# Kernel tuning notes

Hardware: AMD Instinct MI355X
Metric: run time of the kernel (lower is better)

The kernel has to match this reference:

```python
import jax, jax.numpy as jnp
import numpy as np

ROI_SIZE = 7
MAX_BIN_H = 8   # max adaptive-maxpool bin height for crop H <= 37
MAX_BIN_W = 9   # max adaptive-maxpool bin width  for crop W <= 50
SCALE = 0.0625  # 1/16 feature stride


def setup_inputs() -> dict:
    key = jax.random.key(0)
    ks = jax.random.split(key, 12)
    B, C, h, w = 1, 512, 37, 50          # conv5 feature map of a 600x800 image
    N = 512                               # number of ROIs (proposals)
    n_class = 21
    d_in, d_fc = C * ROI_SIZE * ROI_SIZE, 4096
    x = jax.random.normal(ks[0], (B, C, h, w), dtype=jnp.float32)
    # rois in image coordinates (x1, y1, x2, y2), image is 800x600
    x1 = jax.random.uniform(ks[1], (N,), minval=0.0, maxval=700.0)
    y1 = jax.random.uniform(ks[2], (N,), minval=0.0, maxval=500.0)
    bw = jax.random.uniform(ks[3], (N,), minval=16.0, maxval=400.0)
    bh = jax.random.uniform(ks[4], (N,), minval=16.0, maxval=300.0)
    rois = jnp.stack([x1, y1, jnp.minimum(x1 + bw, 799.0), jnp.minimum(y1 + bh, 599.0)], axis=1).astype(jnp.float32)
    roi_index = jnp.zeros((N,), dtype=jnp.int32)  # single image in batch
    W1 = jax.random.normal(ks[5], (d_in, d_fc), dtype=jnp.float32) * 0.01
    b1 = jnp.zeros((d_fc,), dtype=jnp.float32)
    W2 = jax.random.normal(ks[6], (d_fc, d_fc), dtype=jnp.float32) * 0.01
    b2 = jnp.zeros((d_fc,), dtype=jnp.float32)
    Wp = jax.random.normal(ks[7], (d_fc, n_class * 4), dtype=jnp.float32) * 0.001
    bp = jax.random.normal(ks[8], (n_class * 4,), dtype=jnp.float32) * 0.001
    Ws = jax.random.normal(ks[9], (d_fc, n_class), dtype=jnp.float32) * 0.01
    bs = jax.random.normal(ks[10], (n_class,), dtype=jnp.float32) * 0.01
    return dict(x=x, rois=rois, roi_index=roi_index, W1=W1, b1=b1, W2=W2, b2=b2, Wp=Wp, bp=bp, Ws=Ws, bs=bs)


def _roi_pool(x, rois, roi_index):
    """Faithful port of roi_pooling(): per-ROI crop + AdaptiveMaxPool2d(7)."""
    B, C, h, w = x.shape
    S = ROI_SIZE
    coords = jnp.round(rois * SCALE)  # round-half-even, like torch.round
    cx1 = jnp.clip(coords[:, 0], 0, w).astype(jnp.int32)
    cy1 = jnp.clip(coords[:, 1], 0, h).astype(jnp.int32)
    cx2 = jnp.clip(coords[:, 2], 0, w).astype(jnp.int32)
    cy2 = jnp.clip(coords[:, 3], 0, h).astype(jnp.int32)
    bidx = roi_index.astype(jnp.int32)
    roi_stack = jnp.stack([bidx, cx1, cy1, cx2, cy2], axis=1)  # [N,5]

    def pool_one(carry, roi):
        bi, x1i, y1i, x2i, y2i = roi[0], roi[1], roi[2], roi[3], roi[4]
        valid = (x1i < x2i) & (y1i < y2i)
        # torch slicing roi[2]:roi[4]+1 silently truncates at the tensor edge
        x2e = jnp.minimum(x2i, w - 1)
        y2e = jnp.minimum(y2i, h - 1)
        Hc = y2e - y1i + 1
        Wc = x2e - x1i + 1
        i = jnp.arange(S)
        # adaptive max pool bins: [floor(i*H/S), ceil((i+1)*H/S))
        rs = y1i + (i * Hc) // S
        re = y1i + ((i + 1) * Hc + S - 1) // S
        cs = x1i + (i * Wc) // S
        ce = x1i + ((i + 1) * Wc + S - 1) // S
        rows = rs[:, None] + jnp.arange(MAX_BIN_H)          # [S, MBH]
        rmask = rows < re[:, None]
        rows = jnp.clip(rows, 0, h - 1)
        cols = cs[:, None] + jnp.arange(MAX_BIN_W)          # [S, MBW]
        cmask = cols < ce[:, None]
        cols = jnp.clip(cols, 0, w - 1)
        feat = x[bi]                                         # [C, h, w]
        g = feat[:, rows[:, None, :, None], cols[None, :, None, :]]  # [C,S,S,MBH,MBW]
        mask = rmask[:, None, :, None] & cmask[None, :, None, :]     # [S,S,MBH,MBW]
        pooled = jnp.where(mask, g, -jnp.inf).max(axis=(-2, -1))    # [C,S,S]
        pooled = jnp.where(valid, pooled, jnp.zeros_like(pooled))
        return carry, pooled

    _, out = jax.lax.scan(pool_one, None, roi_stack)  # [N, C, S, S]
    return out


def reference(x, rois, roi_index, W1, b1, W2, b2, Wp, bp, Ws, bs):
    pooled = _roi_pool(x, rois, roi_index)            # [N, 512, 7, 7]
    flat = pooled.reshape(pooled.shape[0], -1)        # [N, 25088]
    fc6 = jax.nn.relu(flat @ W1 + b1)                 # [N, 4096]
    fc7 = jax.nn.relu(fc6 @ W2 + b2)                  # [N, 4096]
    roi_class_params = fc7 @ Wp + bp                  # [N, n_class*4]
    roi_scores = fc7 @ Ws + bs                        # [N, n_class]
    return (roi_class_params, roi_scores)
```

## Files before the change

### kernel.cpp

```cpp
#include <hip/hip_runtime.h>
#include <hip/hip_bf16.h>

using f32x4  = float          __attribute__((ext_vector_type(4)));
using bf16x8 = __bf16         __attribute__((ext_vector_type(8)));
using u16x8  = unsigned short __attribute__((ext_vector_type(8)));

#define C_CH 512
#define H_IN 37
#define W_IN 50
#define NPOS 1850
#define NROI 512
#define DIN  25088
#define DFC  4096
#define NPAR 84
#define NCLS 21
#define KS_FC 4
#define KS_HEAD 16

#define PB_X  232
#define PB_WH 2048
#define PB_TOT (PB_X + PB_WH)

__device__ __forceinline__ unsigned pack_bf16x2(float a, float b) {
    __hip_bfloat162 h;
    h.x = __float2bfloat16(a);
    h.y = __float2bfloat16(b);
    return *reinterpret_cast<unsigned*>(&h);
}

__global__ __launch_bounds__(256) void prep_kernel(
        const float* __restrict__ x, float* __restrict__ xt,
        const float* __restrict__ Wp, const float* __restrict__ Ws,
        float* __restrict__ Whp) {
    __shared__ float tile[64][65];
    int b = blockIdx.x;
    int t = threadIdx.x;
    if (b < PB_X) {
        int p0 = (b % 29) * 64;
        int c0 = (b / 29) * 64;
        int tc = t & 63, tr = t >> 6;
#pragma unroll
        for (int i = 0; i < 16; ++i) {
            int r = tr + i * 4;
            int p = p0 + tc;
            float v = 0.f;
            if (p < NPOS) v = x[(size_t)(c0 + r) * NPOS + p];
            tile[r][tc] = v;
        }
        __syncthreads();
#pragma unroll
        for (int i = 0; i < 16; ++i) {
            int rw = tr + i * 4;
            int p = p0 + rw;
            if (p < NPOS) xt[(size_t)p * C_CH + c0 + tc] = tile[tc][rw];
        }
    } else {
        int idx = (b - PB_X) * 256 + t;
        int k = idx >> 7, c = idx & 127;
        float v = 0.f;
        if (c < NPAR) v = Wp[(size_t)k * NPAR + c];
        else if (c < NPAR + NCLS) v = Ws[(size_t)k * NCLS + (c - NPAR)];
        Whp[idx] = v;
    }
}

__global__ __launch_bounds__(256) void roi_pool_kernel(
        const float* __restrict__ xt, const float* __restrict__ rois,
        __hip_bfloat16* __restrict__ pooled) {
    int n = blockIdx.x;
    int t = threadIdx.x;
    float4 rv = reinterpret_cast<const float4*>(rois)[n];
    int x1 = (int)fminf(fmaxf(rintf(rv.x * 0.0625f), 0.f), (float)W_IN);
    int y1 = (int)fminf(fmaxf(rintf(rv.y * 0.0625f), 0.f), (float)H_IN);
    int x2 = (int)fminf(fmaxf(rintf(rv.z * 0.0625f), 0.f), (float)W_IN);
    int y2 = (int)fminf(fmaxf(rintf(rv.w * 0.0625f), 0.f), (float)H_IN);
    bool valid = (x1 < x2) && (y1 < y2);
    unsigned* outp = reinterpret_cast<unsigned*>(pooled) + (size_t)n * (DIN / 2);
    if (!valid) {
        for (int b = 0; b < 49; ++b) outp[b * 256 + t] = 0u;
        return;
    }
    int x2e = min(x2, W_IN - 1), y2e = min(y2, H_IN - 1);
    int Hc = y2e - y1 + 1, Wc = x2e - x1 + 1;
    const float2* base = reinterpret_cast<const float2*>(xt);
    for (int i = 0; i < 7; ++i) {
        int rs = y1 + (i * Hc) / 7;
        int re = y1 + ((i + 1) * Hc + 6) / 7;
        for (int j = 0; j < 7; ++j) {
            int cs = x1 + (j * Wc) / 7;
            int ce = x1 + ((j + 1) * Wc + 6) / 7;
            float m0 = -__builtin_inff(), m1 = -__builtin_inff();
            for (int r = rs; r < re; ++r) {
                const float2* rowp = base + (size_t)r * (W_IN * C_CH / 2) + t;
                for (int c = cs; c < ce; ++c) {
                    float2 v = rowp[c * (C_CH / 2)];
                    m0 = fmaxf(m0, v.x);
                    m1 = fmaxf(m1, v.y);
                }
            }
            outp[(i * 7 + j) * 256 + t] = pack_bf16x2(m0, m1);
        }
    }
}

__device__ __forceinline__ void gload_lds16(const void* src, void* dst) {
    __builtin_amdgcn_global_load_lds(
        (const __attribute__((address_space(1))) void*)src,
        (__attribute__((address_space(3))) void*)dst, 16, 0, 0);
}

__global__ __launch_bounds__(512, 2) void gemm_f32b_kernel(
        const __hip_bfloat16* __restrict__ A,
        const float* __restrict__ Bf,
        float* __restrict__ Cp,
        int N, int lda, int ldbn, int kChunk, int nMT, int nNT, int Mtot,
        int perm) {
    __shared__ __align__(16) char lA[3 * 16384];
    __shared__ __align__(16) char lB[2 * 16384];
    int q = gridDim.x >> 3;
    int bid = (blockIdx.x & 7) * q + (blockIdx.x >> 3);
    int mt = bid % nMT;
    int nt = (bid / nMT) % nNT;
    int ks = bid / (nMT * nNT);
    int m0 = mt * 128, n0 = nt * 128;
    int k0 = ks * kChunk;
    int t = threadIdx.x;
    int lane = t & 63, wid = t >> 6;

    const char* srcA[2]; int offA[2];
#pragma unroll
    for (int i = 0; i < 2; ++i) {
        int p = t * 16 + i * 8192;
        int row = p >> 7;
        int swz = ((row ^ (row >> 3)) & 7) << 4;
        srcA[i] = (const char*)A + ((size_t)(m0 + row) * lda + k0) * 2
                  + ((p & 127) ^ swz);
        offA[i] = p;
    }
    auto stageA = [&](int buf) {
#pragma unroll
        for (int i = 0; i < 2; ++i) {
            gload_lds16(srcA[i], lA + buf * 16384 + offA[i]);
            srcA[i] += 128;
        }
    };

    int n4 = (t & 31) * 4;
    int kq = (t >> 5) * 4;
    int woff[4];
#pragma unroll
    for (int j = 0; j < 4; ++j) {
        int row = n4 + j;
        int swz = ((row ^ (row >> 3)) & 7) << 4;
        woff[j] = row * 128 + ((kq * 2) ^ swz);
    }
    const float* Bbase = Bf + n0 + n4;
    f32x4 v[4];
    auto loadB = [&](int kt) {
        int kb = k0 + kt * 64;
        int rbase = perm ? ((kb & 511) * 49 + (kb >> 9)) : kb;
        int rstr  = perm ? 49 : 1;
#pragma unroll
        for (int p = 0; p < 4; ++p)
            v[p] = *reinterpret_cast<const f32x4*>(
                Bbase + (size_t)(rbase + (kq + p) * rstr) * ldbn);
    };
    auto cvtB = [&](int buf) {
#pragma unroll
        for (int j = 0; j < 4; ++j) {
            uint2 w;
            w.x = pack_bf16x2(v[0][j], v[1][j]);
            w.y = pack_bf16x2(v[2][j], v[3][j]);
            *reinterpret_cast<uint2*>(lB + buf * 16384 + woff[j]) = w;
        }
    };

    int wm = wid >> 2, wn = wid & 3;
    int kb0 = (lane >> 4) << 4;
    int roA[4], roB[2], sA[4], sB[2];
#pragma unroll
    for (int f = 0; f < 4; ++f) {
        int ra = wm * 64 + f * 16 + (lane & 15);
        roA[f] = ra * 128; sA[f] = ((ra ^ (ra >> 3)) & 7) << 4;
    }
#pragma unroll
    for (int f = 0; f < 2; ++f) {
        int rb = wn * 32 + f * 16 + (lane & 15);
        roB[f] = rb * 128; sB[f] = ((rb ^ (rb >> 3)) & 7) << 4;
    }

    f32x4 acc[4][2] = {};
    auto mfmaStep = [&](int aBuf, int bBuf) {
        const char* baseA = lA + aBuf * 16384;
        const char* baseB = lB + bBuf * 16384;
#pragma unroll
        for (int ksub = 0; ksub < 2; ++ksub) {
            int kk = kb0 | (ksub << 6);
            bf16x8 af[4], bfr[2];
#pragma unroll
            for (int f = 0; f < 4; ++f)
                af[f] = *reinterpret_cast<const bf16x8*>(baseA + roA[f] + (kk ^ sA[f]));
#pragma unroll
            for (int f = 0; f < 2; ++f)
                bfr[f] = *reinterpret_cast<const bf16x8*>(baseB + roB[f] + (kk ^ sB[f]));
#pragma unroll
            for (int mf = 0; mf < 4; ++mf)
#pragma unroll
                for (int nf = 0; nf < 2; ++nf)
                    acc[mf][nf] = __builtin_amdgcn_mfma_f32_16x16x32_bf16(
                        af[mf], bfr[nf], acc[mf][nf], 0, 0, 0);
        }
    };

    int nkt = kChunk >> 6;

    stageA(0);
    stageA(1);
    loadB(0);
    cvtB(0);
    loadB(1);
    asm volatile("s_waitcnt vmcnt(4) lgkmcnt(0)\ns_barrier" ::: "memory");

    int aCur = 0, aStage = 2, bCur = 0;
    for (int kt = 0; kt + 2 < nkt; ++kt) {
        stageA(aStage);
        mfmaStep(aCur, bCur);
        cvtB(bCur ^ 1);
        loadB(kt + 2);
        asm volatile("s_waitcnt vmcnt(6) lgkmcnt(0)\ns_barrier" ::: "memory");
        aCur = aCur == 2 ? 0 : aCur + 1;
        aStage = aStage == 2 ? 0 : aStage + 1;
        bCur ^= 1;
    }
    mfmaStep(aCur, bCur);
    cvtB(bCur ^ 1);
    asm volatile("s_waitcnt vmcnt(0) lgkmcnt(0)\ns_barrier" ::: "memory");
    aCur = aCur == 2 ? 0 : aCur + 1;
    bCur ^= 1;
    mfmaStep(aCur, bCur);

    float* outp = Cp + (size_t)ks * Mtot * N;
    int rbase = m0 + wm * 64;
    int cbase = n0 + wn * 32 + (lane & 15);
    int rl = (lane >> 4) * 4;
#pragma unroll
    for (int mf = 0; mf < 4; ++mf)
#pragma unroll
        for (int nf = 0; nf < 2; ++nf)
#pragma unroll
            for (int r = 0; r < 4; ++r)
                outp[(size_t)(rbase + mf * 16 + rl + r) * N + cbase + nf * 16] =
                    acc[mf][nf][r];
}

__global__ __launch_bounds__(256) void reduce_bias_relu_kernel(
        const float* __restrict__ P, const float* __restrict__ bias,
        __hip_bfloat16* __restrict__ out, int MN, int N, int KS) {
    int idx = blockIdx.x * blockDim.x + threadIdx.x;
    int e0 = idx * 4;
    if (e0 >= MN) return;
    f32x4 s = *reinterpret_cast<const f32x4*>(P + e0);
    for (int k = 1; k < KS; ++k)
        s += *reinterpret_cast<const f32x4*>(P + (size_t)k * MN + e0);
    f32x4 b = *reinterpret_cast<const f32x4*>(bias + (e0 & (N - 1)));
    s += b;
    uint2 pk;
    pk.x = pack_bf16x2(fmaxf(s[0], 0.f), fmaxf(s[1], 0.f));
    pk.y = pack_bf16x2(fmaxf(s[2], 0.f), fmaxf(s[3], 0.f));
    *reinterpret_cast<uint2*>(reinterpret_cast<char*>(out) + (size_t)e0 * 2) = pk;
}

__global__ __launch_bounds__(128) void head_reduce_kernel(
        const float* __restrict__ P, const float* __restrict__ bp,
        const float* __restrict__ bs, float* __restrict__ out) {
    int n = blockIdx.x, c = threadIdx.x;
    float s = 0.f;
#pragma unroll
    for (int ks = 0; ks < KS_HEAD; ++ks)
        s += P[(size_t)ks * NROI * 128 + (size_t)n * 128 + c];
    if (c < NPAR)
        out[(size_t)n * NPAR + c] = s + bp[c];
    else if (c < NPAR + NCLS)
        out[(size_t)NROI * NPAR + (size_t)n * NCLS + (c - NPAR)] = s + bs[c - NPAR];
}

extern "C" void kernel_launch(void* const* d_in, const int* in_sizes, int n_in,
                              void* d_out, int out_size, void* d_ws, size_t ws_size,
                              hipStream_t stream) {
    const float* x    = (const float*)d_in[0];
    const float* rois = (const float*)d_in[1];
    const float* W1 = (const float*)d_in[3];
    const float* b1 = (const float*)d_in[4];
    const float* W2 = (const float*)d_in[5];
    const float* b2 = (const float*)d_in[6];
    const float* Wp = (const float*)d_in[7];
    const float* bp = (const float*)d_in[8];
    const float* Ws = (const float*)d_in[9];
    const float* bs = (const float*)d_in[10];
    float* out = (float*)d_out;

    const size_t MB = 1ull << 20;
    char* ws = (char*)d_ws;
    float*          xt     = (float*)(ws + 0);
    __hip_bfloat16* pooled = (__hip_bfloat16*)(ws + 4   * MB);
    float*          Whp    = (float*)(ws + 30  * MB);
    float*          part   = (float*)(ws + 34  * MB);
    __hip_bfloat16* fc6    = (__hip_bfloat16*)(ws + 104 * MB);
    __hip_bfloat16* fc7    = (__hip_bfloat16*)(ws + 109 * MB);

    prep_kernel<<<PB_TOT, 256, 0, stream>>>(x, xt, Wp, Ws, Whp);
    roi_pool_kernel<<<NROI, 256, 0, stream>>>(xt, rois, pooled);

    gemm_f32b_kernel<<<4 * 32 * KS_FC, 512, 0, stream>>>(
        pooled, W1, part, DFC, DIN, DFC, DIN / KS_FC, 4, 32, NROI, 1);
    reduce_bias_relu_kernel<<<2048, 256, 0, stream>>>(part, b1, fc6,
                                                      NROI * DFC, DFC, KS_FC);

    gemm_f32b_kernel<<<4 * 32 * KS_FC, 512, 0, stream>>>(
        fc6, W2, part, DFC, DFC, DFC, DFC / KS_FC, 4, 32, NROI, 0);
    reduce_bias_relu_kernel<<<2048, 256, 0, stream>>>(part, b2, fc7,
                                                      NROI * DFC, DFC, KS_FC);

    gemm_f32b_kernel<<<4 * KS_HEAD, 512, 0, stream>>>(
        fc7, Whp, part, 128, DFC, 128, DFC / KS_HEAD, 4, 1, NROI, 0);
    head_reduce_kernel<<<NROI, 128, 0, stream>>>(part, bp, bs, out);
}
```

Baseline: 368.4 us.

## Add 128x256-tile GEMM kernel for fc6/fc7 to halve activation reloads

Adds a new GEMM kernel with a 128x256 output tile per block (warps arranged 2x4, each computing 64x64) and uses it for the two large FC layers in place of the 128x128 kernel. The aim is to cut how often the bf16 activation tiles are re-read from memory across N tiles, and to raise MFMA work per LDS fragment load. In exchange the grid is halved to 256 blocks (fewer than two blocks per CU), more LDS is used per block, the launch_bounds occupancy hint is dropped, and each thread holds 16 accumulator vectors, which raises register pressure.

```diff
diff --git a/kernel.cpp b/kernel.cpp
--- a/kernel.cpp
+++ b/kernel.cpp
@@ -26,6 +26,12 @@
     h.x = __float2bfloat16(a);
     h.y = __float2bfloat16(b);
     return *reinterpret_cast<unsigned*>(&h);
+}
+
+__device__ __forceinline__ void gload_lds16(const void* src, void* dst) {
+    __builtin_amdgcn_global_load_lds(
+        (const __attribute__((address_space(1))) void*)src,
+        (__attribute__((address_space(3))) void*)dst, 16, 0, 0);
 }
 
 __global__ __launch_bounds__(256) void prep_kernel(
@@ -103,10 +109,147 @@
     }
 }
 
-__device__ __forceinline__ void gload_lds16(const void* src, void* dst) {
-    __builtin_amdgcn_global_load_lds(
-        (const __attribute__((address_space(1))) void*)src,
-        (__attribute__((address_space(3))) void*)dst, 16, 0, 0);
+__global__ __launch_bounds__(512) void gemm_w256_kernel(
+        const __hip_bfloat16* __restrict__ A,
+        const float* __restrict__ Bf,
+        float* __restrict__ Cp,
+        int N, int lda, int ldbn, int kChunk, int nMT, int nNT, int Mtot,
+        int perm) {
+    __shared__ __align__(16) char lA[3 * 16384];
+    __shared__ __align__(16) char lB[2 * 32768];
+    int q = gridDim.x >> 3;
+    int bid = (blockIdx.x & 7) * q + (blockIdx.x >> 3);
+    int mt = bid % nMT;
+    int nt = (bid / nMT) % nNT;
+    int ks = bid / (nMT * nNT);
+    int m0 = mt * 128, n0 = nt * 256;
+    int k0 = ks * kChunk;
+    int t = threadIdx.x;
+    int lane = t & 63, wid = t >> 6;
+
+    const char* srcA[2]; int offA[2];
+#pragma unroll
+    for (int i = 0; i < 2; ++i) {
+        int p = t * 16 + i * 8192;
+        int row = p >> 7;
+        int swz = ((row ^ (row >> 3)) & 7) << 4;
+        srcA[i] = (const char*)A + ((size_t)(m0 + row) * lda + k0) * 2
+                  + ((p & 127) ^ swz);
+        offA[i] = p;
+    }
+    auto stageA = [&](int buf) {
+#pragma unroll
+        for (int i = 0; i < 2; ++i) {
+            gload_lds16(srcA[i], lA + buf * 16384 + offA[i]);
+            srcA[i] += 128;
+        }
+    };
+
+    int n4 = (t & 63) * 4;
+    int k8 = (t >> 6) * 8;
+    int woff[4];
+#pragma unroll
+    for (int j = 0; j < 4; ++j) {
+        int row = n4 + j;
+        int swz = ((row ^ (row >> 3)) & 7) << 4;
+        woff[j] = row * 128 + ((k8 * 2) ^ swz);
+    }
+    const float* Bbase = Bf + n0 + n4;
+    f32x4 v[8];
+    auto loadB = [&](int kt) {
+        int kb = k0 + kt * 64;
+        int rbase = perm ? ((kb & 511) * 49 + (kb >> 9)) : kb;
+        int rstr  = perm ? 49 : 1;
+#pragma unroll
+        for (int p = 0; p < 8; ++p)
+            v[p] = *reinterpret_cast<const f32x4*>(
+                Bbase + (size_t)(rbase + (k8 + p) * rstr) * ldbn);
+    };
+    auto cvtB = [&](int buf) {
+#pragma unroll
+        for (int j = 0; j < 4; ++j) {
+            uint4 w;
+            w.x = pack_bf16x2(v[0][j], v[1][j]);
+            w.y = pack_bf16x2(v[2][j], v[3][j]);
+            w.z = pack_bf16x2(v[4][j], v[5][j]);
+            w.w = pack_bf16x2(v[6][j], v[7][j]);
+            *reinterpret_cast<uint4*>(lB + buf * 32768 + woff[j]) = w;
+        }
+    };
+
+    int wm = wid >> 2, wn = wid & 3;
+    int kb0 = (lane >> 4) << 4;
+    int roA[4], roB[4], sA[4], sB[4];
+#pragma unroll
+    for (int f = 0; f < 4; ++f) {
+        int ra = wm * 64 + f * 16 + (lane & 15);
+        roA[f] = ra * 128; sA[f] = ((ra ^ (ra >> 3)) & 7) << 4;
+        int rb = wn * 64 + f * 16 + (lane & 15);
+        roB[f] = rb * 128; sB[f] = ((rb ^ (rb >> 3)) & 7) << 4;
+    }
+
+    f32x4 acc[4][4] = {};
+    auto mfmaStep = [&](int aBuf, int bBuf) {
+        const char* baseA = lA + aBuf * 16384;
+        const char* baseB = lB + bBuf * 32768;
+#pragma unroll
+        for (int ksub = 0; ksub < 2; ++ksub) {
+            int kk = kb0 | (ksub << 6);
+            bf16x8 af[4], bfr[4];
+#pragma unroll
+            for (int f = 0; f < 4; ++f)
+                af[f] = *reinterpret_cast<const bf16x8*>(baseA + roA[f] + (kk ^ sA[f]));
+#pragma unroll
+            for (int f = 0; f < 4; ++f)
+                bfr[f] = *reinterpret_cast<const bf16x8*>(baseB + roB[f] + (kk ^ sB[f]));
+#pragma unroll
+            for (int mf = 0; mf < 4; ++mf)
+#pragma unroll
+                for (int nf = 0; nf < 4; ++nf)
+                    acc[mf][nf] = __builtin_amdgcn_mfma_f32_16x16x32_bf16(
+                        af[mf], bfr[nf], acc[mf][nf], 0, 0, 0);
+        }
+    };
+
+    int nkt = kChunk >> 6;
+
+    stageA(0);
+    stageA(1);
+    loadB(0);
+    cvtB(0);
+    loadB(1);
+    asm volatile("s_waitcnt vmcnt(8) lgkmcnt(0)\ns_barrier" ::: "memory");
+
+    int aCur = 0, aStage = 2, bCur = 0;
+    for (int kt = 0; kt + 2 < nkt; ++kt) {
+        stageA(aStage);
+        mfmaStep(aCur, bCur);
+        cvtB(bCur ^ 1);
+        loadB(kt + 2);
+        asm volatile("s_waitcnt vmcnt(10) lgkmcnt(0)\ns_barrier" ::: "memory");
+        aCur = aCur == 2 ? 0 : aCur + 1;
+        aStage = aStage == 2 ? 0 : aStage + 1;
+        bCur ^= 1;
+    }
+    mfmaStep(aCur, bCur);
+    cvtB(bCur ^ 1);
+    asm volatile("s_waitcnt vmcnt(0) lgkmcnt(0)\ns_barrier" ::: "memory");
+    aCur = aCur == 2 ? 0 : aCur + 1;
+    bCur ^= 1;
+    mfmaStep(aCur, bCur);
+
+    float* outp = Cp + (size_t)ks * Mtot * N;
+    int rbase = m0 + wm * 64;
+    int cbase = n0 + wn * 64 + (lane & 15);
+    int rl = (lane >> 4) * 4;
+#pragma unroll
+    for (int mf = 0; mf < 4; ++mf)
+#pragma unroll
+        for (int nf = 0; nf < 4; ++nf)
+#pragma unroll
+            for (int r = 0; r < 4; ++r)
+                outp[(size_t)(rbase + mf * 16 + rl + r) * N + cbase + nf * 16] =
+                    acc[mf][nf][r];
 }
 
 __global__ __launch_bounds__(512, 2) void gemm_f32b_kernel(
@@ -311,13 +454,13 @@
     prep_kernel<<<PB_TOT, 256, 0, stream>>>(x, xt, Wp, Ws, Whp);
     roi_pool_kernel<<<NROI, 256, 0, stream>>>(xt, rois, pooled);
 
-    gemm_f32b_kernel<<<4 * 32 * KS_FC, 512, 0, stream>>>(
-        pooled, W1, part, DFC, DIN, DFC, DIN / KS_FC, 4, 32, NROI, 1);
+    gemm_w256_kernel<<<4 * 16 * KS_FC, 512, 0, stream>>>(
+        pooled, W1, part, DFC, DIN, DFC, DIN / KS_FC, 4, 16, NROI, 1);
     reduce_bias_relu_kernel<<<2048, 256, 0, stream>>>(part, b1, fc6,
                                                       NROI * DFC, DFC, KS_FC);
 
-    gemm_f32b_kernel<<<4 * 32 * KS_FC, 512, 0, stream>>>(
-        fc6, W2, part, DFC, DFC, DFC, DFC / KS_FC, 4, 32, NROI, 0);
+    gemm_w256_kernel<<<4 * 16 * KS_FC, 512, 0, stream>>>(
+        fc6, W2, part, DFC, DFC, DFC, DFC / KS_FC, 4, 16, NROI, 0);
     reduce_bias_relu_kernel<<<2048, 256, 0, stream>>>(part, b2, fc7,
                                                       NROI * DFC, DFC, KS_FC);
 
```

Result: slower. 376.9 us (+2.3%).
